# Optimization experiments

Measured on AMD Instinct MI355X. Metric: run time of the kernel, lower is better.

The kernel has to match this reference:

```python
import jax, jax.numpy as jnp
import numpy as np

N = 3072      # num nodes in g
E = 3072      # num edges in g (= num nodes in line graph lg)
E_LG = 6144   # num edges in line graph
F_NODE = 64
F_EDGE = 64
H = 4         # num_heads


def _init_linear(key, fan_in, fan_out):
    k1, k2 = jax.random.split(key)
    bound = 1.0 / np.sqrt(fan_in).astype(np.float32)
    W = jax.random.uniform(k1, (fan_in, fan_out), minval=-bound, maxval=bound, dtype=jnp.float32)
    b = jax.random.uniform(k2, (fan_out,), minval=-bound, maxval=bound, dtype=jnp.float32)
    return W, b


def setup_inputs() -> dict:
    key = jax.random.key(0)
    ks = jax.random.split(key, 12)
    node_inputs = jax.random.normal(ks[0], (N, F_NODE), dtype=jnp.float32)
    edge_inputs = jax.random.normal(ks[1], (E, F_EDGE), dtype=jnp.float32)
    src = jax.random.randint(ks[2], (E,), 0, N)
    dst = jax.random.randint(ks[3], (E,), 0, N)
    lg_src = jax.random.randint(ks[4], (E_LG,), 0, E)
    lg_dst = jax.random.randint(ks[5], (E_LG,), 0, E)
    nqW, nqb = _init_linear(ks[6], F_NODE, H * F_NODE)
    nkW, nkb = _init_linear(ks[7], F_NODE, H)
    nvW, nvb = _init_linear(ks[8], F_NODE, H * F_NODE)
    eqW, eqb = _init_linear(ks[9], F_EDGE, H * F_EDGE)
    ekW, ekb = _init_linear(ks[10], F_EDGE, H)
    evW, evb = _init_linear(ks[11], F_EDGE, H * F_EDGE)
    return dict(node_inputs=node_inputs, edge_inputs=edge_inputs,
                src=src, dst=dst, lg_src=lg_src, lg_dst=lg_dst,
                nqW=nqW, nqb=nqb, nkW=nkW, nkb=nkb, nvW=nvW, nvb=nvb,
                eqW=eqW, eqb=eqb, ekW=ekW, ekb=ekb, evW=evW, evb=evb)


def _self_attention(query, key_t, feats, short_residual):
    # query [H,M,F], key_t [H,M,1], short_residual [M,F]
    # original: softmax((q @ sr^T @ k) / sqrt(F), dim=1)
    # associate as q @ (sr^T @ k) to avoid an [H,M,M] intermediate
    srk = jnp.einsum('mf,hmo->hfo', short_residual, key_t)          # [H,F,1]
    x = jnp.einsum('hmf,hfo->hmo', query, srk) / np.float32(np.sqrt(feats))
    return jax.nn.softmax(x, axis=1)                                 # [H,M,1]


def reference(node_inputs, edge_inputs, src, dst, lg_src, lg_dst,
              nqW, nqb, nkW, nkb, nvW, nvb, eqW, eqb, ekW, ekb, evW, evb):
    # linear projections; torch .view(H,-1,F) on a row-major [M,H*F] tensor
    # is exactly jnp.reshape((H, M, F))
    node_q = (node_inputs @ nqW + nqb).reshape(H, N, F_NODE)
    node_k = (node_inputs @ nkW + nkb).reshape(H, N, 1)
    node_v = (node_inputs @ nvW + nvb).reshape(H, N, F_NODE)
    edge_q = (edge_inputs @ eqW + eqb).reshape(H, E, F_EDGE)
    edge_k = (edge_inputs @ ekW + ekb).reshape(H, E, 1)
    edge_v = (edge_inputs @ evW + evb).reshape(H, E, F_EDGE)

    node_att = _self_attention(node_q, node_k, F_NODE, node_inputs)  # [H,N,1]
    edge_att = _self_attention(edge_q, edge_k, F_EDGE, edge_inputs)  # [H,E,1]

    # scatter per-edge attention scores into dense [H,N,N]
    node_proj = jnp.zeros((H, N, N), jnp.float32).at[:, src, dst].set(edge_att[:, :, 0])
    # line-graph edge e1 -> e2 passes through connecting node dst[e1]
    conn = dst[lg_src]                                               # [E_LG]
    edge_proj = jnp.zeros((H, E, E), jnp.float32).at[:, lg_src, lg_dst].set(node_att[:, conn, 0])

    # dense adjacency masks
    adj_g = jnp.zeros((N, N), jnp.float32).at[src, dst].set(1.0)
    adj_lg = jnp.zeros((E, E), jnp.float32).at[lg_src, lg_dst].set(1.0)

    # message passing, aggregation='sum': (proj * adj) @ value
    node_msg = jnp.einsum('hnm,hmf->hnf', node_proj * adj_g, node_v)   # [H,N,F]
    edge_msg = jnp.einsum('hnm,hmf->hnf', edge_proj * adj_lg, edge_v)  # [H,E,F]

    # head pooling 'mean' (dropout p=0 => identity)
    return node_msg.mean(axis=0), edge_msg.mean(axis=0)
```

## Files before the change

kernel.cpp:

```cpp
#include <hip/hip_runtime.h>

#define N_NODES 3072
#define N_EDGES 3072
#define N_LG    6144
#define F       64
#define H       4

#define OFF_PV   0
#define OFF_SRKP (OFF_PV + 2*H*N_NODES*F)
#define OFF_ATT  (OFF_SRKP + 96*64)
#define OFF_TAB  (OFF_ATT + 2*H*N_NODES)
#define TAB_SZ   (N_NODES * N_NODES)

#define L_SIN   0
#define L_KL    4352
#define L_WK    4608
#define L_BK    4864
#define L_PRED  4868
#define LDS_FLOATS (L_PRED + 256)

__global__ __launch_bounds__(256) void phase1_kernel(
    const float* __restrict__ node_in, const float* __restrict__ edge_in,
    const int* __restrict__ src, const int* __restrict__ dst,
    const int* __restrict__ lg_src, const int* __restrict__ lg_dst,
    const float* __restrict__ nkW, const float* __restrict__ nkb,
    const float* __restrict__ ekW, const float* __restrict__ ekb,
    const float* __restrict__ nvW, const float* __restrict__ nvb,
    const float* __restrict__ evW, const float* __restrict__ evb,
    float* __restrict__ ws, float* __restrict__ out)
{
    const int b = blockIdx.x, t = threadIdx.x;
    __shared__ float lds[LDS_FLOATS];

    if (b < 96) {
        const int tile = b % 48, kind = b / 48;
        const int h = tile / 12, mblk = tile % 12, m0 = mblk * 256, r0 = tile * 64;
        const float* in = kind ? edge_in : node_in;
        const float* Wk = kind ? ekW : nkW;
        const float* bk = kind ? ekb : nkb;
        float* sin_ = lds + L_SIN;
        float* k_lds = lds + L_KL;
        float* wk_s = lds + L_WK;
        float* bk_s = lds + L_BK;
        #pragma unroll
        for (int i = 0; i < 4; ++i) {
            const int idx = t + i * 256;
            const int m = idx >> 4, q = idx & 15;
            float4 v = ((const float4*)(in + (size_t)(r0 + m) * F))[q];
            *(float4*)&sin_[m * 68 + q * 4] = v;
        }
        wk_s[t] = Wk[t];
        if (t < 4) bk_s[t] = bk[t];
        __syncthreads();
        {
            const int rl = t >> 2, c = t & 3;
            float acc = bk_s[c];
            #pragma unroll
            for (int j = 0; j < F; ++j) acc += sin_[rl * 68 + j] * wk_s[j * 4 + c];
            k_lds[t] = acc;
        }
        __syncthreads();
        {
            const int c = t >> 6, f = t & 63;
            float acc = 0.f;
            const float* base = in + (size_t)(m0 + c * 64) * F + f;
            #pragma unroll
            for (int mp = 0; mp < 64; ++mp) acc += base[(size_t)mp * F] * k_lds[c * 64 + mp];
            float* pred = lds + L_PRED;
            pred[t] = acc;
            __syncthreads();
            if (t < 64)
                ws[OFF_SRKP + ((kind * H + h) * 12 + mblk) * 64 + t]
                    = pred[t] + pred[64 + t] + pred[128 + t] + pred[192 + t];
        }
    } else if (b < 288) {
        const int p = b - 96;
        const int kind = p / 96, m0 = (p % 96) * 32;
        const float* in = kind ? edge_in : node_in;
        const float* W  = kind ? evW : nvW;
        const float* bv = kind ? evb : nvb;
        float* sin_ = lds + L_SIN;
        #pragma unroll
        for (int i = 0; i < 2; ++i) {
            const int idx = t + i * 256;
            const int m = idx >> 4, q = idx & 15;
            float4 v = ((const float4*)(in + (size_t)(m0 + m) * F))[q];
            *(float4*)&sin_[m * 68 + q * 4] = v;
        }
        __syncthreads();
        float acc[32];
        const float b0 = bv[t];
        #pragma unroll
        for (int r = 0; r < 32; ++r) acc[r] = b0;
        #pragma unroll
        for (int k4 = 0; k4 < 16; ++k4) {
            const float w0 = W[(k4 * 4 + 0) * 256 + t];
            const float w1 = W[(k4 * 4 + 1) * 256 + t];
            const float w2 = W[(k4 * 4 + 2) * 256 + t];
            const float w3 = W[(k4 * 4 + 3) * 256 + t];
            #pragma unroll
            for (int r = 0; r < 32; ++r) {
                float4 v = *(const float4*)&sin_[r * 68 + k4 * 4];
                acc[r] = fmaf(v.x, w0, fmaf(v.y, w1, fmaf(v.z, w2, fmaf(v.w, w3, acc[r]))));
            }
        }
        float* V = ws + OFF_PV + (size_t)kind * H * N_NODES * F;
        #pragma unroll
        for (int r = 0; r < 32; ++r)
            V[(size_t)(m0 + r) * 256 + t] = acc[r];
    } else if (b < 324) {
        const int task = (b - 288) * 256 + t;
        int* T_g  = (int*)(ws + OFF_TAB);
        int* T_lg = T_g + TAB_SZ;
        if (task < N_EDGES) {
            atomicMax(&T_g[src[task] * N_NODES + dst[task]], task);
        } else {
            const int l = task - N_EDGES;
            atomicMax(&T_lg[lg_src[l] * N_NODES + lg_dst[l]], l);
        }
    } else {
        ((float4*)out)[(b - 324) * 256 + t] = make_float4(0.f, 0.f, 0.f, 0.f);
    }
}

__global__ __launch_bounds__(1024) void att_kernel(
    const float* __restrict__ node_in, const float* __restrict__ edge_in,
    const float* __restrict__ nqW, const float* __restrict__ nqb,
    const float* __restrict__ eqW, const float* __restrict__ eqb,
    float* __restrict__ ws)
{
    const int h = blockIdx.x, kind = blockIdx.y, tid = threadIdx.x;
    const float* in = kind ? edge_in : node_in;
    const float* Wq = kind ? eqW : nqW;
    const float* bq = kind ? eqb : nqb;
    float* att = ws + OFF_ATT + (kind * H + h) * N_NODES;
    __shared__ float s_srk[F];
    __shared__ float s_w[256];
    __shared__ float s_beff[4];
    __shared__ float sred[16];
    if (tid < F) {
        float s = 0.f;
        #pragma unroll
        for (int mb = 0; mb < 12; ++mb)
            s += ws[OFF_SRKP + ((kind * H + h) * 12 + mb) * 64 + tid];
        s_srk[tid] = s;
    }
    __syncthreads();
    if (tid < 256) {
        const int c4 = tid >> 6, j = tid & 63;
        float we = 0.f;
        #pragma unroll
        for (int f = 0; f < F; ++f) we += Wq[j * 256 + c4 * 64 + f] * s_srk[f];
        s_w[c4 * 64 + j] = we;
    } else if (tid < 260) {
        const int c4 = tid - 256;
        float be = 0.f;
        #pragma unroll
        for (int f = 0; f < F; ++f) be += bq[c4 * 64 + f] * s_srk[f];
        s_beff[c4] = be;
    }
    __syncthreads();
    float x[3];
    float mx = -1e30f;
    #pragma unroll
    for (int j = 0; j < 3; ++j) {
        const int m = tid * 3 + j;
        const int row = h * 768 + (m >> 2);
        const int c4 = m & 3;
        const float4* q4 = (const float4*)(in + (size_t)row * F);
        const float* w = s_w + c4 * 64;
        float a = 0.f;
        #pragma unroll
        for (int i = 0; i < 16; ++i) {
            float4 v = q4[i];
            a += v.x * w[i * 4] + v.y * w[i * 4 + 1] + v.z * w[i * 4 + 2] + v.w * w[i * 4 + 3];
        }
        x[j] = (a + s_beff[c4]) * 0.125f;
        mx = fmaxf(mx, x[j]);
    }
    #pragma unroll
    for (int o = 1; o < 64; o <<= 1) mx = fmaxf(mx, __shfl_xor(mx, o));
    const int wid = tid >> 6, lane = tid & 63;
    if (lane == 0) sred[wid] = mx;
    __syncthreads();
    if (tid == 0) { float m2 = sred[0]; for (int i = 1; i < 16; ++i) m2 = fmaxf(m2, sred[i]); sred[0] = m2; }
    __syncthreads();
    mx = sred[0];
    __syncthreads();
    float s = 0.f;
    #pragma unroll
    for (int j = 0; j < 3; ++j) { x[j] = __expf(x[j] - mx); s += x[j]; }
    #pragma unroll
    for (int o = 1; o < 64; o <<= 1) s += __shfl_xor(s, o);
    if (lane == 0) sred[wid] = s;
    __syncthreads();
    if (tid == 0) { float t = 0.f; for (int i = 0; i < 16; ++i) t += sred[i]; sred[0] = t; }
    __syncthreads();
    const float inv = 1.0f / sred[0];
    #pragma unroll
    for (int j = 0; j < 3; ++j) att[tid * 3 + j] = x[j] * inv;
}

__global__ __launch_bounds__(256) void scatter_kernel(
    const int* __restrict__ src, const int* __restrict__ dst,
    const int* __restrict__ lg_src, const int* __restrict__ lg_dst,
    const float* __restrict__ ws,
    float* __restrict__ out)
{
    const int* T_g  = (const int*)(ws + OFF_TAB);
    const int* T_lg = T_g + TAB_SZ;
    const int g = threadIdx.x >> 6, f = threadIdx.x & 63;
    const int task = blockIdx.x * 4 + g;
    if (task < N_EDGES) {
        const int e = task;
        const int s = src[e], d = dst[e];
        if (T_g[s * N_NODES + d] != e) return;
        const float* att = ws + OFF_ATT + H * N_NODES;
        const float* V   = ws + OFF_PV;
        float acc = 0.f;
        #pragma unroll
        for (int h = 0; h < H; ++h)
            acc += att[h * N_EDGES + e] * V[(size_t)h * N_NODES * F + (size_t)d * F + f];
        atomicAdd(&out[s * F + f], 0.25f * acc);
    } else {
        const int l = task - N_EDGES;
        const int e1 = lg_src[l], e2 = lg_dst[l];
        if (T_lg[e1 * N_NODES + e2] != l) return;
        const int conn = dst[e1];
        const float* att = ws + OFF_ATT;
        const float* V   = ws + OFF_PV + (size_t)H * N_EDGES * F;
        float acc = 0.f;
        #pragma unroll
        for (int h = 0; h < H; ++h)
            acc += att[h * N_NODES + conn] * V[(size_t)h * N_EDGES * F + (size_t)e2 * F + f];
        atomicAdd(&out[N_NODES * F + e1 * F + f], 0.25f * acc);
    }
}

extern "C" void kernel_launch(void* const* d_in, const int* in_sizes, int n_in,
                              void* d_out, int out_size, void* d_ws, size_t ws_size,
                              hipStream_t stream)
{
    const float* node_in = (const float*)d_in[0];
    const float* edge_in = (const float*)d_in[1];
    const int* src    = (const int*)d_in[2];
    const int* dst    = (const int*)d_in[3];
    const int* lg_src = (const int*)d_in[4];
    const int* lg_dst = (const int*)d_in[5];
    const float* nqW = (const float*)d_in[6];  const float* nqb = (const float*)d_in[7];
    const float* nkW = (const float*)d_in[8];  const float* nkb = (const float*)d_in[9];
    const float* nvW = (const float*)d_in[10]; const float* nvb = (const float*)d_in[11];
    const float* eqW = (const float*)d_in[12]; const float* eqb = (const float*)d_in[13];
    const float* ekW = (const float*)d_in[14]; const float* ekb = (const float*)d_in[15];
    const float* evW = (const float*)d_in[16]; const float* evb = (const float*)d_in[17];

    float* ws  = (float*)d_ws;
    float* out = (float*)d_out;

    hipLaunchKernelGGL(phase1_kernel, dim3(708), dim3(256), 0, stream,
                       node_in, edge_in, src, dst, lg_src, lg_dst,
                       nkW, nkb, ekW, ekb, nvW, nvb, evW, evb, ws, out);
    hipLaunchKernelGGL(att_kernel, dim3(H, 2), dim3(1024), 0, stream,
                       node_in, edge_in, nqW, nqb, eqW, eqb, ws);
    hipLaunchKernelGGL(scatter_kernel, dim3((N_EDGES + N_LG) / 4), dim3(256), 0, stream,
                       src, dst, lg_src, lg_dst, ws, out);
}
```

Before: 140.9 us.

## Fuse attention computation into phase-1 kernel, dropping separate att launch

The separate attention-softmax kernel is removed. Its work now runs in 8 blocks of the first kernel, one per (kind, head), and each of those blocks computes its own key projection, the sr^T·k reduction, the effective query weights and the softmax. This drops a kernel launch and the partial-sum workspace round trip. In exchange, those 8 blocks each do a long serial 768-step reduction and 12 rows per thread, so they may become the critical path of the fused kernel.

Result: no change. 140.6 us (-0.2%).

```diff
diff --git a/kernel.cpp b/kernel.cpp
--- a/kernel.cpp
+++ b/kernel.cpp
@@ -7,79 +7,125 @@
 #define H       4
 
 #define OFF_PV   0
-#define OFF_SRKP (OFF_PV + 2*H*N_NODES*F)
-#define OFF_ATT  (OFF_SRKP + 96*64)
+#define OFF_ATT  (OFF_PV + 2*H*N_NODES*F)
 #define OFF_TAB  (OFF_ATT + 2*H*N_NODES)
 #define TAB_SZ   (N_NODES * N_NODES)
 
-#define L_SIN   0
-#define L_KL    4352
-#define L_WK    4608
-#define L_BK    4864
-#define L_PRED  4868
-#define LDS_FLOATS (L_PRED + 256)
-
-__global__ __launch_bounds__(256) void phase1_kernel(
+__global__ __launch_bounds__(256) void fused_kernel(
     const float* __restrict__ node_in, const float* __restrict__ edge_in,
     const int* __restrict__ src, const int* __restrict__ dst,
     const int* __restrict__ lg_src, const int* __restrict__ lg_dst,
+    const float* __restrict__ nqW, const float* __restrict__ nqb,
     const float* __restrict__ nkW, const float* __restrict__ nkb,
+    const float* __restrict__ nvW, const float* __restrict__ nvb,
+    const float* __restrict__ eqW, const float* __restrict__ eqb,
     const float* __restrict__ ekW, const float* __restrict__ ekb,
-    const float* __restrict__ nvW, const float* __restrict__ nvb,
     const float* __restrict__ evW, const float* __restrict__ evb,
     float* __restrict__ ws, float* __restrict__ out)
 {
     const int b = blockIdx.x, t = threadIdx.x;
-    __shared__ float lds[LDS_FLOATS];
-
-    if (b < 96) {
-        const int tile = b % 48, kind = b / 48;
-        const int h = tile / 12, mblk = tile % 12, m0 = mblk * 256, r0 = tile * 64;
+
+    if (b < 8) {
+        const int h = b & 3, kind = b >> 2;
         const float* in = kind ? edge_in : node_in;
         const float* Wk = kind ? ekW : nkW;
         const float* bk = kind ? ekb : nkb;
-        float* sin_ = lds + L_SIN;
-        float* k_lds = lds + L_KL;
-        float* wk_s = lds + L_WK;
-        float* bk_s = lds + L_BK;
-        #pragma unroll
-        for (int i = 0; i < 4; ++i) {
-            const int idx = t + i * 256;
-            const int m = idx >> 4, q = idx & 15;
-            float4 v = ((const float4*)(in + (size_t)(r0 + m) * F))[q];
-            *(float4*)&sin_[m * 68 + q * 4] = v;
-        }
+        const float* Wq = kind ? eqW : nqW;
+        const float* bq = kind ? eqb : nqb;
+        float* att = ws + OFF_ATT + (kind * H + h) * N_NODES;
+
+        __shared__ float k_lds[3072];
+        __shared__ float wk_s[256];
+        __shared__ float bk_s[4];
+        __shared__ float s_srk[64];
+        __shared__ float s_w[256];
+        __shared__ float s_beff[4];
+        __shared__ float sred[8];
+        __shared__ float pred[256];
+
         wk_s[t] = Wk[t];
         if (t < 4) bk_s[t] = bk[t];
         __syncthreads();
-        {
-            const int rl = t >> 2, c = t & 3;
+        #pragma unroll
+        for (int j = 0; j < 12; ++j) {
+            const int m = t + 256 * j;
+            const int c = m & 3;
+            const float4* row4 = (const float4*)(in + (size_t)(h * 768 + (m >> 2)) * F);
             float acc = bk_s[c];
             #pragma unroll
-            for (int j = 0; j < F; ++j) acc += sin_[rl * 68 + j] * wk_s[j * 4 + c];
-            k_lds[t] = acc;
+            for (int i = 0; i < 16; ++i) {
+                float4 v = row4[i];
+                acc += v.x * wk_s[(i * 4 + 0) * 4 + c] + v.y * wk_s[(i * 4 + 1) * 4 + c]
+                     + v.z * wk_s[(i * 4 + 2) * 4 + c] + v.w * wk_s[(i * 4 + 3) * 4 + c];
+            }
+            k_lds[m] = acc;
         }
         __syncthreads();
         {
             const int c = t >> 6, f = t & 63;
             float acc = 0.f;
-            const float* base = in + (size_t)(m0 + c * 64) * F + f;
-            #pragma unroll
-            for (int mp = 0; mp < 64; ++mp) acc += base[(size_t)mp * F] * k_lds[c * 64 + mp];
-            float* pred = lds + L_PRED;
+            const float* base = in + (size_t)(c * 768) * F + f;
+            for (int mp = 0; mp < 768; ++mp)
+                acc += base[(size_t)mp * F] * k_lds[c * 768 + mp];
             pred[t] = acc;
             __syncthreads();
-            if (t < 64)
-                ws[OFF_SRKP + ((kind * H + h) * 12 + mblk) * 64 + t]
-                    = pred[t] + pred[64 + t] + pred[128 + t] + pred[192 + t];
-        }
-    } else if (b < 288) {
-        const int p = b - 96;
+            if (t < 64) s_srk[t] = pred[t] + pred[64 + t] + pred[128 + t] + pred[192 + t];
+        }
+        __syncthreads();
+        {
+            const int c4 = t >> 6, j = t & 63;
+            float we = 0.f;
+            #pragma unroll
+            for (int f = 0; f < F; ++f) we += Wq[j * 256 + c4 * 64 + f] * s_srk[f];
+            s_w[c4 * 64 + j] = we;
+        }
+        if (t < 4) {
+            float be = 0.f;
+            #pragma unroll
+            for (int f = 0; f < F; ++f) be += bq[t * 64 + f] * s_srk[f];
+            s_beff[t] = be;
+        }
+        __syncthreads();
+        float x[12];
+        float mx = -1e30f;
+        #pragma unroll
+        for (int j = 0; j < 12; ++j) {
+            const int m = t + 256 * j;
+            const int c4 = m & 3;
+            const float4* q4 = (const float4*)(in + (size_t)(h * 768 + (m >> 2)) * F);
+            const float* w = s_w + c4 * 64;
+            float a = 0.f;
+            #pragma unroll
+            for (int i = 0; i < 16; ++i) {
+                float4 v = q4[i];
+                a += v.x * w[i * 4] + v.y * w[i * 4 + 1] + v.z * w[i * 4 + 2] + v.w * w[i * 4 + 3];
+            }
+            x[j] = (a + s_beff[c4]) * 0.125f;
+            mx = fmaxf(mx, x[j]);
+        }
+        const int wid = t >> 6, lane = t & 63;
+        #pragma unroll
+        for (int o = 1; o < 64; o <<= 1) mx = fmaxf(mx, __shfl_xor(mx, o));
+        if (lane == 0) sred[wid] = mx;
+        __syncthreads();
+        mx = fmaxf(fmaxf(sred[0], sred[1]), fmaxf(sred[2], sred[3]));
+        float s = 0.f;
+        #pragma unroll
+        for (int j = 0; j < 12; ++j) { x[j] = __expf(x[j] - mx); s += x[j]; }
+        #pragma unroll
+        for (int o = 1; o < 64; o <<= 1) s += __shfl_xor(s, o);
+        if (lane == 0) sred[4 + wid] = s;
+        __syncthreads();
+        const float inv = 1.0f / (sred[4] + sred[5] + sred[6] + sred[7]);
+        #pragma unroll
+        for (int j = 0; j < 12; ++j) att[t + 256 * j] = x[j] * inv;
+    } else if (b < 200) {
+        const int p = b - 8;
         const int kind = p / 96, m0 = (p % 96) * 32;
         const float* in = kind ? edge_in : node_in;
         const float* W  = kind ? evW : nvW;
         const float* bv = kind ? evb : nvb;
-        float* sin_ = lds + L_SIN;
+        __shared__ float sin_[32 * 68];
         #pragma unroll
         for (int i = 0; i < 2; ++i) {
             const int idx = t + i * 256;
@@ -108,8 +154,8 @@
         #pragma unroll
         for (int r = 0; r < 32; ++r)
             V[(size_t)(m0 + r) * 256 + t] = acc[r];
-    } else if (b < 324) {
-        const int task = (b - 288) * 256 + t;
+    } else if (b < 236) {
+        const int task = (b - 200) * 256 + t;
         int* T_g  = (int*)(ws + OFF_TAB);
         int* T_lg = T_g + TAB_SZ;
         if (task < N_EDGES) {
@@ -119,86 +165,8 @@
             atomicMax(&T_lg[lg_src[l] * N_NODES + lg_dst[l]], l);
         }
     } else {
-        ((float4*)out)[(b - 324) * 256 + t] = make_float4(0.f, 0.f, 0.f, 0.f);
+        ((float4*)out)[(b - 236) * 256 + t] = make_float4(0.f, 0.f, 0.f, 0.f);
     }
-}
-
-__global__ __launch_bounds__(1024) void att_kernel(
-    const float* __restrict__ node_in, const float* __restrict__ edge_in,
-    const float* __restrict__ nqW, const float* __restrict__ nqb,
-    const float* __restrict__ eqW, const float* __restrict__ eqb,
-    float* __restrict__ ws)
-{
-    const int h = blockIdx.x, kind = blockIdx.y, tid = threadIdx.x;
-    const float* in = kind ? edge_in : node_in;
-    const float* Wq = kind ? eqW : nqW;
-    const float* bq = kind ? eqb : nqb;
-    float* att = ws + OFF_ATT + (kind * H + h) * N_NODES;
-    __shared__ float s_srk[F];
-    __shared__ float s_w[256];
-    __shared__ float s_beff[4];
-    __shared__ float sred[16];
-    if (tid < F) {
-        float s = 0.f;
-        #pragma unroll
-        for (int mb = 0; mb < 12; ++mb)
-            s += ws[OFF_SRKP + ((kind * H + h) * 12 + mb) * 64 + tid];
-        s_srk[tid] = s;
-    }
-    __syncthreads();
-    if (tid < 256) {
-        const int c4 = tid >> 6, j = tid & 63;
-        float we = 0.f;
-        #pragma unroll
-        for (int f = 0; f < F; ++f) we += Wq[j * 256 + c4 * 64 + f] * s_srk[f];
-        s_w[c4 * 64 + j] = we;
-    } else if (tid < 260) {
-        const int c4 = tid - 256;
-        float be = 0.f;
-        #pragma unroll
-        for (int f = 0; f < F; ++f) be += bq[c4 * 64 + f] * s_srk[f];
-        s_beff[c4] = be;
-    }
-    __syncthreads();
-    float x[3];
-    float mx = -1e30f;
-    #pragma unroll
-    for (int j = 0; j < 3; ++j) {
-        const int m = tid * 3 + j;
-        const int row = h * 768 + (m >> 2);
-        const int c4 = m & 3;
-        const float4* q4 = (const float4*)(in + (size_t)row * F);
-        const float* w = s_w + c4 * 64;
-        float a = 0.f;
-        #pragma unroll
-        for (int i = 0; i < 16; ++i) {
-            float4 v = q4[i];
-            a += v.x * w[i * 4] + v.y * w[i * 4 + 1] + v.z * w[i * 4 + 2] + v.w * w[i * 4 + 3];
-        }
-        x[j] = (a + s_beff[c4]) * 0.125f;
-        mx = fmaxf(mx, x[j]);
-    }
-    #pragma unroll
-    for (int o = 1; o < 64; o <<= 1) mx = fmaxf(mx, __shfl_xor(mx, o));
-    const int wid = tid >> 6, lane = tid & 63;
-    if (lane == 0) sred[wid] = mx;
-    __syncthreads();
-    if (tid == 0) { float m2 = sred[0]; for (int i = 1; i < 16; ++i) m2 = fmaxf(m2, sred[i]); sred[0] = m2; }
-    __syncthreads();
-    mx = sred[0];
-    __syncthreads();
-    float s = 0.f;
-    #pragma unroll
-    for (int j = 0; j < 3; ++j) { x[j] = __expf(x[j] - mx); s += x[j]; }
-    #pragma unroll
-    for (int o = 1; o < 64; o <<= 1) s += __shfl_xor(s, o);
-    if (lane == 0) sred[wid] = s;
-    __syncthreads();
-    if (tid == 0) { float t = 0.f; for (int i = 0; i < 16; ++i) t += sred[i]; sred[0] = t; }
-    __syncthreads();
-    const float inv = 1.0f / sred[0];
-    #pragma unroll
-    for (int j = 0; j < 3; ++j) att[tid * 3 + j] = x[j] * inv;
 }
 
 __global__ __launch_bounds__(256) void scatter_kernel(
@@ -257,11 +225,10 @@
     float* ws  = (float*)d_ws;
     float* out = (float*)d_out;
 
-    hipLaunchKernelGGL(phase1_kernel, dim3(708), dim3(256), 0, stream,
+    hipLaunchKernelGGL(fused_kernel, dim3(620), dim3(256), 0, stream,
                        node_in, edge_in, src, dst, lg_src, lg_dst,
-                       nkW, nkb, ekW, ekb, nvW, nvb, evW, evb, ws, out);
-    hipLaunchKernelGGL(att_kernel, dim3(H, 2), dim3(1024), 0, stream,
-                       node_in, edge_in, nqW, nqb, eqW, eqb, ws);
+                       nqW, nqb, nkW, nkb, nvW, nvb,
+                       eqW, eqb, ekW, ekb, evW, evb, ws, out);
     hipLaunchKernelGGL(scatter_kernel, dim3((N_EDGES + N_LG) / 4), dim3(256), 0, stream,
                        src, dst, lg_src, lg_dst, ws, out);
 }
```
